# Kernel tuning notes

Hardware: AMD Instinct MI355X
Metric: run time of the kernel (lower is better)

## Reference

```python
import jax, jax.numpy as jnp
import numpy as np

K = 15          # k_point_level
EPS = 1e-5      # BatchNorm eps
NEG = 0.2       # LeakyReLU slope


def _lrelu(y):
    return jnp.where(y > 0, y, NEG * y)


def _knn_idx(x, k):
    # x: [N, C, P] -> idx [N, P, k] of nearest points (incl. self) by -||xi-xj||^2 topk
    inner = -2.0 * jnp.einsum('ncp,ncq->npq', x, x)
    xx = jnp.sum(x * x, axis=1)                      # [N, P]
    pd = -xx[:, :, None] - inner - xx[:, None, :]    # [N, P, P]
    return jax.lax.top_k(pd, k)[1]


def _edge_feature(x, k):
    # x: [N, C, P] -> [N, P, k, 2C] = concat(neigh - center, center)
    N = x.shape[0]
    idx = _knn_idx(x, k)                             # [N, P, k]
    xt = jnp.transpose(x, (0, 2, 1))                 # [N, P, C]
    neigh = xt[jnp.arange(N)[:, None, None], idx]    # [N, P, k, C]
    center = jnp.broadcast_to(xt[:, :, None, :], neigh.shape)
    return jnp.concatenate([neigh - center, center], axis=-1)


def _edge_block(x, W, gamma, beta, k):
    # EdgeConv: gather -> 1x1 conv -> BN (batch stats) -> LeakyReLU -> max over k
    f = _edge_feature(x, k)                          # [N, P, k, 2C]
    y = jnp.einsum('npkc,oc->npko', f, W)
    m = jnp.mean(y, axis=(0, 1, 2))
    v = jnp.var(y, axis=(0, 1, 2))
    y = (y - m) * jax.lax.rsqrt(v + EPS) * gamma + beta
    y = jnp.max(_lrelu(y), axis=2)                   # [N, P, O]
    return jnp.transpose(y, (0, 2, 1))               # [N, O, P]


def _forward(x, W1, g1, b1, W2, g2, b2, W3, g3, b3, W4, g4, b4,
             W5, g5, b5, Wl1, g6, b6, Wl2, bl2, g7, b7, Wl3, bl3):
    x1 = _edge_block(x, W1, g1, b1, K)               # [N, 64, P]
    x2 = _edge_block(x1, W2, g2, b2, K)              # [N, 64, P]
    x3 = _edge_block(x2, W3, g3, b3, K)              # [N, 128, P]
    x4 = _edge_block(x3, W4, g4, b4, K)              # [N, 256, P]
    xc = jnp.concatenate([x1, x2, x3, x4], axis=1)   # [N, 512, P]
    y = jnp.einsum('ncp,oc->npo', xc, W5)            # [N, P, emb]
    m = jnp.mean(y, axis=(0, 1)); v = jnp.var(y, axis=(0, 1))
    y = _lrelu((y - m) * jax.lax.rsqrt(v + EPS) * g5 + b5)
    h = jnp.concatenate([jnp.max(y, axis=1), jnp.mean(y, axis=1)], axis=1)  # [N, 2*emb]
    h = h @ Wl1.T
    m = jnp.mean(h, axis=0); v = jnp.var(h, axis=0)
    h = _lrelu((h - m) * jax.lax.rsqrt(v + EPS) * g6 + b6)
    h = h @ Wl2.T + bl2
    m = jnp.mean(h, axis=0); v = jnp.var(h, axis=0)
    h = _lrelu((h - m) * jax.lax.rsqrt(v + EPS) * g7 + b7)
    logits = h @ Wl3.T + bl3
    return jax.nn.log_softmax(logits, axis=1)


def setup_inputs() -> dict:
    key = jax.random.key(0)
    ks = iter(jax.random.split(key, 16))
    N, P, EMB, NC = 2048, 32, 1024, 800

    def w(k, o, i):
        return jax.random.normal(k, (o, i), jnp.float32) / np.sqrt(i)

    d = {
        'x': jax.random.normal(next(ks), (N, 3, P), jnp.float32),
        'info_point_set': jnp.zeros((1,), jnp.float32),
        'W1': w(next(ks), 64, 6),   'g1': jnp.ones(64),  'b1': jnp.zeros(64),
        'W2': w(next(ks), 64, 128), 'g2': jnp.ones(64),  'b2': jnp.zeros(64),
        'W3': w(next(ks), 128, 128),'g3': jnp.ones(128), 'b3': jnp.zeros(128),
        'W4': w(next(ks), 256, 256),'g4': jnp.ones(256), 'b4': jnp.zeros(256),
        'W5': w(next(ks), EMB, 512),'g5': jnp.ones(EMB), 'b5': jnp.zeros(EMB),
        'Wl1': w(next(ks), 512, 2 * EMB), 'g6': jnp.ones(512), 'b6': jnp.zeros(512),
        'Wl2': w(next(ks), 256, 512), 'bl2': jnp.zeros(256),
        'g7': jnp.ones(256), 'b7': jnp.zeros(256),
        'Wl3': w(next(ks), NC, 256), 'bl3': jnp.zeros(NC),
    }
    return d


def reference(x, info_point_set, W1, g1, b1, W2, g2, b2, W3, g3, b3,
              W4, g4, b4, W5, g5, b5, Wl1, g6, b6, Wl2, bl2, g7, b7, Wl3, bl3):
    # info_point_set unused: args.k + args.k_global == 0 path (dynamic KNN graph).
    return _forward(x, W1, g1, b1, W2, g2, b2, W3, g3, b3, W4, g4, b4,
                    W5, g5, b5, Wl1, g6, b6, Wl2, bl2, g7, b7, Wl3, bl3)
```

## Files before the change

kernel.cpp:

```cpp
#include <hip/hip_runtime.h>
#include <hip/hip_bf16.h>
#include <cstdint>
#include <cstddef>

#define NPTS 2048
#define P 32
#define KNN_K 15
#define LRELU_NEG 0.2f
#define BN_EPS 1e-5f

__device__ __forceinline__ float lrelu(float x) { return x > 0.f ? x : LRELU_NEG * x; }

__device__ __forceinline__ unsigned short f2bf(float x) {
    union { float f; unsigned u; } uu; uu.f = x;
    unsigned r = uu.u + 0x7fffu + ((uu.u >> 16) & 1u);
    return (unsigned short)(r >> 16);
}
__device__ __forceinline__ float bf2f(unsigned short b) {
    union { unsigned u; float f; } uu; uu.u = ((unsigned)b) << 16;
    return uu.f;
}

typedef short bf16x8 __attribute__((ext_vector_type(8)));
typedef float f32x4  __attribute__((ext_vector_type(4)));

template<int C>
__global__ __launch_bounds__(64) void knn_kernel(const float* __restrict__ xin, int cloudStride,
                                                 unsigned char* __restrict__ idx)
{
    const int n = blockIdx.x, t = threadIdx.x;
    __shared__ float xs[C][P];
    __shared__ float xx[P];
    __shared__ float pd[P][P + 1];
    const float* xp = xin + (size_t)n * cloudStride;
    for (int i = t; i < C * P; i += 64) xs[i / P][i % P] = xp[i];
    __syncthreads();
    if (t < P) { float s = 0.f; for (int c = 0; c < C; ++c) { float v = xs[c][t]; s = fmaf(v, v, s); } xx[t] = s; }
    __syncthreads();
    for (int i = t; i < P * P; i += 64) {
        int p = i >> 5, q = i & 31;
        float d = 0.f;
        for (int c = 0; c < C; ++c) d = fmaf(xs[c][p], xs[c][q], d);
        pd[p][q] = 2.f * d - xx[p] - xx[q];
    }
    __syncthreads();
    if (t < P) {
        for (int j = 0; j < KNN_K; ++j) {
            float best = -INFINITY; int bq = 0;
            for (int q = 0; q < P; ++q) { float v = pd[t][q]; if (v > best) { best = v; bq = q; } }
            idx[(size_t)n * (P * KNN_K) + t * KNN_K + j] = (unsigned char)bq;
            pd[t][bq] = -INFINITY;
        }
    }
}

__global__ __launch_bounds__(256) void build_wcat_kernel(const float* __restrict__ W, float* __restrict__ wt,
                                                         int C, int O, int NCHUNK)
{
    int i = blockIdx.x * 256 + threadIdx.x;
    int tot = C * 2 * O;
    if (i >= tot) return;
    int c = i / (2 * O), col = i % (2 * O);
    int O2C = 2 * O / NCHUNK, OC = O / NCHUNK;
    int chunk = col / O2C, cl = col % O2C;
    float v;
    if (cl < OC) { int o = chunk * OC + cl; v = W[(size_t)o * 2 * C + c]; }
    else { int o = chunk * OC + cl - OC; v = W[(size_t)o * 2 * C + C + c] - W[(size_t)o * 2 * C + c]; }
    wt[i] = v;
}

__global__ __launch_bounds__(256) void pack_wcat_direct(const float* __restrict__ W,
                                                        unsigned short* __restrict__ wpk,
                                                        int C, int O, int NCHUNK)
{
    const int TOTC = 2 * O, NTT = TOTC / 16;
    const int O2C = TOTC / NCHUNK, OC = O / NCHUNK;
    int i = blockIdx.x * 256 + threadIdx.x;
    if (i >= C * TOTC) return;
    int j = i & 7, lane = (i >> 3) & 63, rest = i >> 9;
    int ntg = rest % NTT, kb = rest / NTT;
    int k = kb * 32 + (lane >> 4) * 8 + j;
    int col = ntg * 16 + (lane & 15);
    int chunk = col / O2C, cl = col % O2C;
    float v;
    if (cl < OC) { int o = chunk * OC + cl; v = W[(size_t)o * 2 * C + k]; }
    else         { int o = chunk * OC + cl - OC; v = W[(size_t)o * 2 * C + C + k] - W[(size_t)o * 2 * C + k]; }
    unsigned short hi = f2bf(v);
    wpk[(size_t)rest * 1024 + lane * 8 + j] = hi;
    wpk[(size_t)rest * 1024 + 512 + lane * 8 + j] = f2bf(v - bf2f(hi));
}

__global__ __launch_bounds__(256) void pack_wfc_kernel(const float* __restrict__ W,
                                                       unsigned short* __restrict__ wpk,
                                                       int Kk, int Nn, int NTT)
{
    int i = blockIdx.x * 256 + threadIdx.x;
    if (i >= NTT * 16 * Kk) return;
    int j = i & 7, lane = (i >> 3) & 63, rest = i >> 9;
    int ntg = rest % NTT, kb = rest / NTT;
    int k = kb * 32 + (lane >> 4) * 8 + j;
    int col = ntg * 16 + (lane & 15);
    float v = (col < Nn) ? W[(size_t)col * Kk + k] : 0.f;
    unsigned short hi = f2bf(v);
    wpk[(size_t)rest * 1024 + lane * 8 + j] = hi;
    wpk[(size_t)rest * 1024 + 512 + lane * 8 + j] = f2bf(v - bf2f(hi));
}

template<int C, int O, int NCHUNK, bool OUT>
__global__ __launch_bounds__(256) void edge_pass_kernel(
    const float* __restrict__ xin, int cloudStride,
    const float* __restrict__ wt,
    const unsigned char* __restrict__ idx,
    const float* __restrict__ st,
    float* __restrict__ xcout,
    float* __restrict__ partS, float* __restrict__ partQ)
{
    constexpr int TOTC = 2 * O;
    constexpr int O2C = TOTC / NCHUNK;
    constexpr int OC  = O / NCHUNK;
    constexpr int TPC = (O2C >= 256) ? 1 : (256 / O2C);
    constexpr int CPT = (O2C > 256) ? (O2C / 256) : 1;
    constexpr int PP  = P / TPC;
    constexpr int TPO = 256 / OC;
    constexpr int PPo = P / TPO;
    const int n = blockIdx.x, t = threadIdx.x;

    __shared__ float xs[C][P];
    __shared__ float gh[P * O2C];
    __shared__ unsigned char idl[P * KNN_K];
    __shared__ float red[2][256];

    const float* xp = xin + (size_t)n * cloudStride;
    for (int i = t; i < C * P; i += 256) xs[i / P][i % P] = xp[i];
    for (int i = t; i < P * KNN_K; i += 256) idl[i] = idx[(size_t)n * (P * KNN_K) + i];

    const int col = (O2C >= 256) ? t : (t % O2C);
    const int p0  = ((O2C >= 256) ? 0 : (t / O2C)) * PP;
    const int o   = t % OC;
    const int p0c = (t / OC) * PPo;

    for (int chunk = 0; chunk < NCHUNK; ++chunk) {
        __syncthreads();
        {
            float acc[CPT][PP];
            #pragma unroll
            for (int j = 0; j < CPT; ++j)
                #pragma unroll
                for (int p = 0; p < PP; ++p) acc[j][p] = 0.f;
            for (int c = 0; c < C; ++c) {
                float w[CPT];
                #pragma unroll
                for (int j = 0; j < CPT; ++j) w[j] = wt[(size_t)c * TOTC + chunk * O2C + col + j * 256];
                #pragma unroll
                for (int p = 0; p < PP; ++p) {
                    float xv = xs[c][p0 + p];
                    #pragma unroll
                    for (int j = 0; j < CPT; ++j) acc[j][p] = fmaf(w[j], xv, acc[j][p]);
                }
            }
            #pragma unroll
            for (int j = 0; j < CPT; ++j)
                #pragma unroll
                for (int p = 0; p < PP; ++p) gh[(p0 + p) * O2C + col + j * 256] = acc[j][p];
        }
        __syncthreads();

        if constexpr (!OUT) {
            float ssum = 0.f, ssq = 0.f;
            #pragma unroll
            for (int p = 0; p < PPo; ++p) {
                const int pp = p0c + p;
                const float g = gh[pp * O2C + OC + o];
                #pragma unroll
                for (int k = 0; k < KNN_K; ++k) {
                    const int q = idl[pp * KNN_K + k];
                    float yv = gh[q * O2C + o] + g;
                    ssum += yv; ssq += yv * yv;
                }
            }
            red[0][t] = ssum; red[1][t] = ssq;
            __syncthreads();
            if (t < OC) {
                float S = 0.f, Q = 0.f;
                #pragma unroll
                for (int j = 0; j < TPO; ++j) { S += red[0][t + j * OC]; Q += red[1][t + j * OC]; }
                partS[(size_t)(chunk * OC + t) * 2048 + n] = S;
                partQ[(size_t)(chunk * OC + t) * 2048 + n] = Q;
            }
        } else {
            const float s = st[chunk * OC + o], sh = st[1024 + chunk * OC + o];
            float rbuf[PPo];
            #pragma unroll
            for (int p = 0; p < PPo; ++p) {
                const int pp = p0c + p;
                const float g = gh[pp * O2C + OC + o];
                float mx = -INFINITY, mn = INFINITY;
                #pragma unroll
                for (int k = 0; k < KNN_K; ++k) {
                    const int q = idl[pp * KNN_K + k];
                    float yv = gh[q * O2C + o] + g;
                    mx = fmaxf(mx, yv); mn = fminf(mn, yv);
                }
                rbuf[p] = lrelu(fmaf(s, (s >= 0.f ? mx : mn), sh));
            }
            __syncthreads();
            #pragma unroll
            for (int p = 0; p < PPo; ++p) gh[o * (P + 1) + p0c + p] = rbuf[p];
            __syncthreads();
            for (int i = t; i < OC * P; i += 256)
                xcout[(size_t)n * (512 * P) + chunk * OC * P + i] = gh[(i / P) * (P + 1) + (i % P)];
        }
    }
}

template<int C, int O, bool OUT>
__global__ __launch_bounds__(256) void edge_mfma_kernel(
    const float* __restrict__ xin, int cloudStride,
    const unsigned short* __restrict__ wpk,
    const unsigned char* __restrict__ idx,
    const float* __restrict__ st,
    float* __restrict__ xcout,
    float* __restrict__ partS, float* __restrict__ partQ)
{
    constexpr int TOTC  = 2 * O;
    constexpr int O2C   = (TOTC > 256) ? 256 : TOTC;
    constexpr int NCHUNK= TOTC / O2C;
    constexpr int OC    = O2C / 2;
    constexpr int NTW   = O2C / 64;
    constexpr int KB    = C / 32;
    constexpr int NTT   = TOTC / 16;
    constexpr int AS    = C + 8;
    constexpr int GHS   = O2C + 4;
    constexpr int TPO   = 256 / OC;
    constexpr int PPo   = P / TPO;

    const int n = blockIdx.x, t = threadIdx.x;
    const int w = t >> 6, l = t & 63;
    const int lg = l >> 4, lm = l & 15;

    __shared__ unsigned short Ah[P * AS];
    __shared__ unsigned short Al[P * AS];
    __shared__ float gh[P * GHS];
    __shared__ unsigned char idl[P * KNN_K];

    const float* xp = xin + (size_t)n * cloudStride;
    for (int i = t; i < C * P; i += 256) {
        int c = i / P, p = i % P;
        float v = xp[i];
        unsigned short hi = f2bf(v);
        Ah[p * AS + c] = hi;
        Al[p * AS + c] = f2bf(v - bf2f(hi));
    }
    for (int i = t; i < P * KNN_K; i += 256) idl[i] = idx[(size_t)n * (P * KNN_K) + i];
    __syncthreads();

    const int o = t % OC;
    const int p0c = (t / OC) * PPo;

    for (int chunk = 0; chunk < NCHUNK; ++chunk) {
        f32x4 acc[2][NTW];
        #pragma unroll
        for (int mt = 0; mt < 2; ++mt)
            #pragma unroll
            for (int nt = 0; nt < NTW; ++nt) acc[mt][nt] = (f32x4)0.f;

        #pragma unroll
        for (int kb = 0; kb < KB; ++kb) {
            bf16x8 a_h[2], a_l[2];
            #pragma unroll
            for (int mt = 0; mt < 2; ++mt) {
                int row = mt * 16 + lm;
                a_h[mt] = *(const bf16x8*)&Ah[row * AS + kb * 32 + lg * 8];
                a_l[mt] = *(const bf16x8*)&Al[row * AS + kb * 32 + lg * 8];
            }
            #pragma unroll
            for (int nt = 0; nt < NTW; ++nt) {
                int ntg = chunk * (O2C / 16) + w * NTW + nt;
                const unsigned short* bp = wpk + (size_t)(kb * NTT + ntg) * 1024 + (size_t)l * 8;
                bf16x8 Bh = *(const bf16x8*)bp;
                bf16x8 Bl = *(const bf16x8*)(bp + 512);
                #pragma unroll
                for (int mt = 0; mt < 2; ++mt) {
                    acc[mt][nt] = __builtin_amdgcn_mfma_f32_16x16x32_bf16(a_h[mt], Bl, acc[mt][nt], 0, 0, 0);
                    acc[mt][nt] = __builtin_amdgcn_mfma_f32_16x16x32_bf16(a_l[mt], Bh, acc[mt][nt], 0, 0, 0);
                    acc[mt][nt] = __builtin_amdgcn_mfma_f32_16x16x32_bf16(a_h[mt], Bh, acc[mt][nt], 0, 0, 0);
                }
            }
        }
        __syncthreads();
        #pragma unroll
        for (int mt = 0; mt < 2; ++mt)
            #pragma unroll
            for (int nt = 0; nt < NTW; ++nt) {
                int colb = (w * NTW + nt) * 16 + lm;
                #pragma unroll
                for (int r = 0; r < 4; ++r)
                    gh[(mt * 16 + lg * 4 + r) * GHS + colb] = acc[mt][nt][r];
            }
        __syncthreads();

        if constexpr (!OUT) {
            float ssum = 0.f, ssq = 0.f;
            #pragma unroll
            for (int p = 0; p < PPo; ++p) {
                const int pp = p0c + p;
                const float g = gh[pp * GHS + OC + o];
                #pragma unroll
                for (int k = 0; k < KNN_K; ++k) {
                    const int q = idl[pp * KNN_K + k];
                    float yv = gh[q * GHS + o] + g;
                    ssum += yv; ssq += yv * yv;
                }
            }
            __syncthreads();
            gh[t] = ssum; gh[256 + t] = ssq;
            __syncthreads();
            if (t < OC) {
                float S = 0.f, Q = 0.f;
                #pragma unroll
                for (int j = 0; j < TPO; ++j) { S += gh[t + j * OC]; Q += gh[256 + t + j * OC]; }
                partS[(size_t)(chunk * OC + t) * 2048 + n] = S;
                partQ[(size_t)(chunk * OC + t) * 2048 + n] = Q;
            }
        } else {
            const float s = st[chunk * OC + o], sh = st[1024 + chunk * OC + o];
            float rbuf[PPo];
            #pragma unroll
            for (int p = 0; p < PPo; ++p) {
                const int pp = p0c + p;
                const float g = gh[pp * GHS + OC + o];
                float mx = -INFINITY, mn = INFINITY;
                #pragma unroll
                for (int k = 0; k < KNN_K; ++k) {
                    const int q = idl[pp * KNN_K + k];
                    float yv = gh[q * GHS + o] + g;
                    mx = fmaxf(mx, yv); mn = fminf(mn, yv);
                }
                rbuf[p] = lrelu(fmaf(s, (s >= 0.f ? mx : mn), sh));
            }
            __syncthreads();
            #pragma unroll
            for (int p = 0; p < PPo; ++p) gh[o * (P + 1) + p0c + p] = rbuf[p];
            __syncthreads();
            for (int i = t; i < OC * P; i += 256)
                xcout[(size_t)n * (512 * P) + chunk * OC * P + i] = gh[(i / P) * (P + 1) + (i % P)];
        }
    }
}

__global__ __launch_bounds__(256) void reduce_stats_kernel(const float* __restrict__ partS,
                                                           const float* __restrict__ partQ,
                                                           const float* __restrict__ gamma,
                                                           const float* __restrict__ beta,
                                                           float* __restrict__ st, int nparts, float inv_count)
{
    const int o = blockIdx.x, t = threadIdx.x;
    __shared__ float rs[256], rq[256];
    float S = 0.f, Q = 0.f;
    for (int i = t; i < nparts; i += 256) { S += partS[(size_t)o * 2048 + i]; Q += partQ[(size_t)o * 2048 + i]; }
    rs[t] = S; rq[t] = Q; __syncthreads();
    for (int w = 128; w > 0; w >>= 1) { if (t < w) { rs[t] += rs[t + w]; rq[t] += rq[t + w]; } __syncthreads(); }
    if (t == 0) {
        float m = rs[0] * inv_count;
        float v = fmaxf(rq[0] * inv_count - m * m, 0.f);
        float s = gamma[o] * rsqrtf(v + BN_EPS);
        st[o] = s;
        st[1024 + o] = fmaf(-m, s, beta[o]);
    }
}

__global__ __launch_bounds__(256) void pack_w5_kernel(const float* __restrict__ W5, unsigned short* __restrict__ wp)
{
    int i = blockIdx.x * 256 + threadIdx.x;
    if (i >= (1 << 19)) return;
    int j = i & 7, lane = (i >> 3) & 63, nt = (i >> 9) & 63, kb = i >> 15;
    int c = kb * 32 + (lane >> 4) * 8 + j;
    int o = nt * 16 + (lane & 15);
    float f = W5[(size_t)o * 512 + c];
    unsigned short hi = f2bf(f);
    unsigned short lo = f2bf(f - bf2f(hi));
    size_t base = (size_t)(kb * 64 + nt) * 2 * 512 + (size_t)lane * 8 + j;
    wp[base] = hi;
    wp[base + 512] = lo;
}

__global__ __launch_bounds__(512) void conv5_store_kernel(
    const float* xc, const unsigned short* __restrict__ wpack,
    unsigned short* y5,
    float* __restrict__ partS, float* __restrict__ partQ)
{
    const int b = blockIdx.x;
    const int t = threadIdx.x;
    const int w = t >> 6, l = t & 63;
    const int lg = l >> 4, lm = l & 15;

    __shared__ unsigned short Ah[2][64][40];
    __shared__ unsigned short Al[2][64][40];

    f32x4 acc[4][8];
    #pragma unroll
    for (int mt = 0; mt < 4; ++mt)
        #pragma unroll
        for (int nt = 0; nt < 8; ++nt) acc[mt][nt] = (f32x4)0.f;

    const float* xbase = xc + (size_t)(b * 2) * (512 * P);

    const int sp4    = t & 7;
    const int schalf = (t >> 3) & 15;
    const int scloud = (t >> 7) & 1;
    const bool sact  = t < 256;

    auto stage = [&](int kb, int buf) {
        if (sact) {
            const float* src = xbase + (size_t)scloud * (512 * P)
                             + (size_t)(kb * 32 + 2 * schalf) * P + sp4 * 4;
            const float4 v0 = *(const float4*)src;
            const float4 v1 = *(const float4*)(src + P);
            const int r0 = scloud * 32 + sp4 * 4;
            #pragma unroll
            for (int e = 0; e < 4; ++e) {
                float a0 = (&v0.x)[e], a1 = (&v1.x)[e];
                unsigned short h0 = f2bf(a0), h1 = f2bf(a1);
                unsigned short l0 = f2bf(a0 - bf2f(h0)), l1 = f2bf(a1 - bf2f(h1));
                *(unsigned*)&Ah[buf][r0 + e][2 * schalf] = (unsigned)h0 | ((unsigned)h1 << 16);
                *(unsigned*)&Al[buf][r0 + e][2 * schalf] = (unsigned)l0 | ((unsigned)l1 << 16);
            }
        }
    };

    stage(0, 0);
    int cur = 0;
    for (int kb = 0; kb < 16; ++kb) {
        __syncthreads();
        if (kb + 1 < 16) stage(kb + 1, cur ^ 1);

        bf16x8 a_h[4], a_l[4];
        #pragma unroll
        for (int mt = 0; mt < 4; ++mt) {
            int row = mt * 16 + lm;
            a_h[mt] = *(const bf16x8*)&Ah[cur][row][lg * 8];
            a_l[mt] = *(const bf16x8*)&Al[cur][row][lg * 8];
        }
        #pragma unroll
        for (int nt = 0; nt < 8; ++nt) {
            const int ntg = w * 8 + nt;
            const unsigned short* bp = wpack + (size_t)(kb * 64 + ntg) * 2 * 512 + (size_t)l * 8;
            bf16x8 Bh = *(const bf16x8*)bp;
            bf16x8 Bl = *(const bf16x8*)(bp + 512);
            #pragma unroll
            for (int mt = 0; mt < 4; ++mt) {
                acc[mt][nt] = __builtin_amdgcn_mfma_f32_16x16x32_bf16(a_h[mt], Bl, acc[mt][nt], 0, 0, 0);
                acc[mt][nt] = __builtin_amdgcn_mfma_f32_16x16x32_bf16(a_l[mt], Bh, acc[mt][nt], 0, 0, 0);
                acc[mt][nt] = __builtin_amdgcn_mfma_f32_16x16x32_bf16(a_h[mt], Bh, acc[mt][nt], 0, 0, 0);
            }
        }
        cur ^= 1;
    }
    __syncthreads();

    #pragma unroll
    for (int nt = 0; nt < 8; ++nt) {
        float s = 0.f, q = 0.f;
        #pragma unroll
        for (int mt = 0; mt < 4; ++mt)
            #pragma unroll
            for (int r = 0; r < 4; ++r) { float v = acc[mt][nt][r]; s += v; q = fmaf(v, v, q); }
        s += __shfl_xor(s, 16); q += __shfl_xor(q, 16);
        s += __shfl_xor(s, 32); q += __shfl_xor(q, 32);
        if (l < 16) {
            int o = w * 128 + nt * 16 + lm;
            partS[(size_t)o * 2048 + b] = s;
            partQ[(size_t)o * 2048 + b] = q;
        }
        #pragma unroll
        for (int mt = 0; mt < 4; ++mt) {
            unsigned p0 = (unsigned)f2bf(acc[mt][nt][0]) | ((unsigned)f2bf(acc[mt][nt][1]) << 16);
            unsigned p1 = (unsigned)f2bf(acc[mt][nt][2]) | ((unsigned)f2bf(acc[mt][nt][3]) << 16);
            size_t off = ((((size_t)b * 8 + w) * 8 + nt) * 4 + mt) * 64 + l;
            ((uint2*)y5)[off] = make_uint2(p0, p1);
        }
    }
}

__global__ __launch_bounds__(512) void conv5_finish_kernel(
    const unsigned short* __restrict__ y5, const float* __restrict__ st, float* __restrict__ h)
{
    const int b = blockIdx.x, t = threadIdx.x;
    const int w = t >> 6, l = t & 63, lm = l & 15;
    #pragma unroll
    for (int nt = 0; nt < 8; ++nt) {
        const int o = w * 128 + nt * 16 + lm;
        const float sc = st[o], sh = st[1024 + o];
        #pragma unroll
        for (int cloud = 0; cloud < 2; ++cloud) {
            float mx = -INFINITY, sm = 0.f;
            #pragma unroll
            for (int half = 0; half < 2; ++half) {
                const int mt = cloud * 2 + half;
                uint2 pk = ((const uint2*)y5)[((((size_t)b * 8 + w) * 8 + nt) * 4 + mt) * 64 + l];
                #pragma unroll
                for (int r = 0; r < 4; ++r) {
                    unsigned word = (r < 2) ? pk.x : pk.y;
                    unsigned short bits = (unsigned short)((r & 1) ? (word >> 16) : (word & 0xffff));
                    float v = lrelu(fmaf(sc, bf2f(bits), sh));
                    mx = fmaxf(mx, v); sm += v;
                }
            }
            mx = fmaxf(mx, __shfl_xor(mx, 16)); sm += __shfl_xor(sm, 16);
            mx = fmaxf(mx, __shfl_xor(mx, 32)); sm += __shfl_xor(sm, 32);
            if (l < 16) {
                const int n = b * 2 + cloud;
                h[(size_t)n * 2048 + o] = mx;
                h[(size_t)n * 2048 + 1024 + o] = sm * (1.f / 32.f);
            }
        }
    }
}

template<bool BNIN, bool STATS>
__global__ __launch_bounds__(256) void gemm_mfma_nt(
    const float* __restrict__ A, const unsigned short* __restrict__ wpk,
    const float* __restrict__ stbn, const float* __restrict__ bias,
    float* __restrict__ Cc, float* __restrict__ partS, float* __restrict__ partQ,
    int Nn, int NTT, int Kk)
{
    const int o0 = blockIdx.x * 64;
    const int m0 = blockIdx.y * 64;
    const int t = threadIdx.x;
    const int w = t >> 6, l = t & 63;
    const int lg = l >> 4, lm = l & 15;

    __shared__ unsigned short Ah[2][64][40];
    __shared__ unsigned short Al[2][64][40];

    f32x4 acc[4];
    #pragma unroll
    for (int mt = 0; mt < 4; ++mt) acc[mt] = (f32x4)0.f;

    const int srow = t >> 3;
    const int sk4  = (t & 7) * 4;

    auto stage = [&](int kb, int buf) {
        const float* src = A + (size_t)(m0 + srow) * Kk + kb * 32 + sk4;
        float4 v0 = *(const float4*)src;
        float4 v1 = *(const float4*)(src + (size_t)32 * Kk);
        if (BNIN) {
            const float4 s4 = *(const float4*)(stbn + kb * 32 + sk4);
            const float4 t4 = *(const float4*)(stbn + 1024 + kb * 32 + sk4);
            #pragma unroll
            for (int e = 0; e < 4; ++e) {
                (&v0.x)[e] = lrelu(fmaf((&s4.x)[e], (&v0.x)[e], (&t4.x)[e]));
                (&v1.x)[e] = lrelu(fmaf((&s4.x)[e], (&v1.x)[e], (&t4.x)[e]));
            }
        }
        #pragma unroll
        for (int e = 0; e < 4; e += 2) {
            float a0 = (&v0.x)[e], a1 = (&v0.x)[e + 1];
            unsigned short h0 = f2bf(a0), h1 = f2bf(a1);
            *(unsigned*)&Ah[buf][srow][sk4 + e] = (unsigned)h0 | ((unsigned)h1 << 16);
            *(unsigned*)&Al[buf][srow][sk4 + e] =
                (unsigned)f2bf(a0 - bf2f(h0)) | ((unsigned)f2bf(a1 - bf2f(h1)) << 16);
            float b0 = (&v1.x)[e], b1 = (&v1.x)[e + 1];
            unsigned short g0 = f2bf(b0), g1 = f2bf(b1);
            *(unsigned*)&Ah[buf][srow + 32][sk4 + e] = (unsigned)g0 | ((unsigned)g1 << 16);
            *(unsigned*)&Al[buf][srow + 32][sk4 + e] =
                (unsigned)f2bf(b0 - bf2f(g0)) | ((unsigned)f2bf(b1 - bf2f(g1)) << 16);
        }
    };

    const int KB = Kk >> 5;
    stage(0, 0);
    int cur = 0;
    const int ntg = blockIdx.x * 4 + w;
    for (int kb = 0; kb < KB; ++kb) {
        __syncthreads();
        if (kb + 1 < KB) stage(kb + 1, cur ^ 1);
        bf16x8 a_h[4], a_l[4];
        #pragma unroll
        for (int mt = 0; mt < 4; ++mt) {
            a_h[mt] = *(const bf16x8*)&Ah[cur][mt * 16 + lm][lg * 8];
            a_l[mt] = *(const bf16x8*)&Al[cur][mt * 16 + lm][lg * 8];
        }
        const unsigned short* bp = wpk + ((size_t)kb * NTT + ntg) * 1024 + (size_t)l * 8;
        bf16x8 Bh = *(const bf16x8*)bp;
        bf16x8 Bl = *(const bf16x8*)(bp + 512);
        #pragma unroll
        for (int mt = 0; mt < 4; ++mt) {
            acc[mt] = __builtin_amdgcn_mfma_f32_16x16x32_bf16(a_h[mt], Bl, acc[mt], 0, 0, 0);
            acc[mt] = __builtin_amdgcn_mfma_f32_16x16x32_bf16(a_l[mt], Bh, acc[mt], 0, 0, 0);
            acc[mt] = __builtin_amdgcn_mfma_f32_16x16x32_bf16(a_h[mt], Bh, acc[mt], 0, 0, 0);
        }
        cur ^= 1;
    }

    const int col = o0 + w * 16 + lm;
    const bool cok = col < Nn;
    const float bv = (bias != nullptr && cok) ? bias[col] : 0.f;
    float s = 0.f, q = 0.f;
    #pragma unroll
    for (int mt = 0; mt < 4; ++mt) {
        #pragma unroll
        for (int r = 0; r < 4; ++r) {
            float v = acc[mt][r] + bv;
            if (STATS) { s += v; q = fmaf(v, v, q); }
            if (cok) Cc[(size_t)(m0 + mt * 16 + lg * 4 + r) * Nn + col] = v;
        }
    }
    if (STATS) {
        s += __shfl_xor(s, 16); q += __shfl_xor(q, 16);
        s += __shfl_xor(s, 32); q += __shfl_xor(q, 32);
        if (l < 16 && cok) {
            partS[(size_t)col * 2048 + blockIdx.y] = s;
            partQ[(size_t)col * 2048 + blockIdx.y] = q;
        }
    }
}

__global__ __launch_bounds__(256) void logsoftmax_kernel(float* __restrict__ out)
{
    const int n = blockIdx.x, t = threadIdx.x;
    float* row = out + (size_t)n * 800;
    __shared__ float red[256];
    float v[4];
    float mx = -INFINITY;
    #pragma unroll
    for (int j = 0; j < 4; ++j) {
        int i = t + j * 256;
        v[j] = (i < 800) ? row[i] : -INFINITY;
        mx = fmaxf(mx, v[j]);
    }
    red[t] = mx; __syncthreads();
    for (int w = 128; w > 0; w >>= 1) { if (t < w) red[t] = fmaxf(red[t], red[t + w]); __syncthreads(); }
    const float m = red[0]; __syncthreads();
    float s = 0.f;
    #pragma unroll
    for (int j = 0; j < 4; ++j) { int i = t + j * 256; if (i < 800) s += expf(v[j] - m); }
    red[t] = s; __syncthreads();
    for (int w = 128; w > 0; w >>= 1) { if (t < w) red[t] += red[t + w]; __syncthreads(); }
    const float lg = m + logf(red[0]);
    #pragma unroll
    for (int j = 0; j < 4; ++j) { int i = t + j * 256; if (i < 800) row[i] = v[j] - lg; }
}

extern "C" void kernel_launch(void* const* d_in, const int* in_sizes, int n_in,
                              void* d_out, int out_size, void* d_ws, size_t ws_size,
                              hipStream_t stream)
{
    (void)in_sizes; (void)n_in; (void)out_size; (void)ws_size;
    const float* x   = (const float*)d_in[0];
    const float* W1  = (const float*)d_in[2];
    const float* g1  = (const float*)d_in[3];
    const float* b1  = (const float*)d_in[4];
    const float* W2  = (const float*)d_in[5];
    const float* g2  = (const float*)d_in[6];
    const float* b2  = (const float*)d_in[7];
    const float* W3  = (const float*)d_in[8];
    const float* g3  = (const float*)d_in[9];
    const float* b3  = (const float*)d_in[10];
    const float* W4  = (const float*)d_in[11];
    const float* g4  = (const float*)d_in[12];
    const float* b4  = (const float*)d_in[13];
    const float* W5  = (const float*)d_in[14];
    const float* g5  = (const float*)d_in[15];
    const float* b5  = (const float*)d_in[16];
    const float* Wl1 = (const float*)d_in[17];
    const float* g6  = (const float*)d_in[18];
    const float* b6  = (const float*)d_in[19];
    const float* Wl2 = (const float*)d_in[20];
    const float* bl2 = (const float*)d_in[21];
    const float* g7  = (const float*)d_in[22];
    const float* b7  = (const float*)d_in[23];
    const float* Wl3 = (const float*)d_in[24];
    const float* bl3 = (const float*)d_in[25];

    char* ws = (char*)d_ws;
    size_t off = 0;
    auto alloc = [&](size_t bytes) -> void* {
        void* p = ws + off; off += (bytes + 255) & ~(size_t)255; return p;
    };
    float*          xc    = (float*)alloc((size_t)NPTS * 512 * P * 4);
    unsigned char*  idx   = (unsigned char*)alloc((size_t)NPTS * P * KNN_K);
    float*          partS = (float*)alloc((size_t)1024 * 2048 * 4);
    float*          partQ = (float*)alloc((size_t)1024 * 2048 * 4);
    float*          st    = (float*)alloc(2048 * 4);
    float*          wt    = (float*)alloc((size_t)512 * 1024 * 4);
    unsigned short* wpk   = (unsigned short*)alloc((size_t)128 * 512 * 2 * 2);
    unsigned short* fcpk  = (unsigned short*)alloc((size_t)512 * 2048 * 2 * 2);
    float*          h     = (float*)alloc((size_t)2048 * 2048 * 4);
    float*          h1p   = (float*)alloc((size_t)2048 * 512 * 4);
    unsigned short* y5 = (unsigned short*)xc;
    float* h2p = h + 1048576;

    const float inv_edge = 1.f / (float)(NPTS * P * KNN_K);

    knn_kernel<3><<<NPTS, 64, 0, stream>>>(x, 3 * P, idx);
    build_wcat_kernel<<<(3 * 128 + 255) / 256, 256, 0, stream>>>(W1, wt, 3, 64, 1);
    edge_pass_kernel<3, 64, 1, false><<<NPTS, 256, 0, stream>>>(x, 3 * P, wt, idx, nullptr, nullptr, partS, partQ);
    reduce_stats_kernel<<<64, 256, 0, stream>>>(partS, partQ, g1, b1, st, 2048, inv_edge);
    edge_pass_kernel<3, 64, 1, true><<<NPTS, 256, 0, stream>>>(x, 3 * P, wt, idx, st, xc + 0 * P, nullptr, nullptr);

    knn_kernel<64><<<NPTS, 64, 0, stream>>>(xc, 512 * P, idx);
    pack_wcat_direct<<<(64 * 128 + 255) / 256, 256, 0, stream>>>(W2, wpk, 64, 64, 1);
    edge_mfma_kernel<64, 64, false><<<NPTS, 256, 0, stream>>>(xc, 512 * P, wpk, idx, nullptr, nullptr, partS, partQ);
    reduce_stats_kernel<<<64, 256, 0, stream>>>(partS, partQ, g2, b2, st, 2048, inv_edge);
    edge_mfma_kernel<64, 64, true><<<NPTS, 256, 0, stream>>>(xc, 512 * P, wpk, idx, st, xc + 64 * P, nullptr, nullptr);

    knn_kernel<64><<<NPTS, 64, 0, stream>>>(xc + 64 * P, 512 * P, idx);
    pack_wcat_direct<<<(64 * 256 + 255) / 256, 256, 0, stream>>>(W3, wpk, 64, 128, 1);
    edge_mfma_kernel<64, 128, false><<<NPTS, 256, 0, stream>>>(xc + 64 * P, 512 * P, wpk, idx, nullptr, nullptr, partS, partQ);
    reduce_stats_kernel<<<128, 256, 0, stream>>>(partS, partQ, g3, b3, st, 2048, inv_edge);
    edge_mfma_kernel<64, 128, true><<<NPTS, 256, 0, stream>>>(xc + 64 * P, 512 * P, wpk, idx, st, xc + 128 * P, nullptr, nullptr);

    knn_kernel<128><<<NPTS, 64, 0, stream>>>(xc + 128 * P, 512 * P, idx);
    pack_wcat_direct<<<(128 * 512 + 255) / 256, 256, 0, stream>>>(W4, wpk, 128, 256, 2);
    edge_mfma_kernel<128, 256, false><<<NPTS, 256, 0, stream>>>(xc + 128 * P, 512 * P, wpk, idx, nullptr, nullptr, partS, partQ);
    reduce_stats_kernel<<<256, 256, 0, stream>>>(partS, partQ, g4, b4, st, 2048, inv_edge);
    edge_mfma_kernel<128, 256, true><<<NPTS, 256, 0, stream>>>(xc + 128 * P, 512 * P, wpk, idx, st, xc + 256 * P, nullptr, nullptr);

    pack_w5_kernel<<<2048, 256, 0, stream>>>(W5, (unsigned short*)wt);
    conv5_store_kernel<<<1024, 512, 0, stream>>>(xc, (const unsigned short*)wt, y5, partS, partQ);
    reduce_stats_kernel<<<1024, 256, 0, stream>>>(partS, partQ, g5, b5, st, 1024, 1.f / 65536.f);
    conv5_finish_kernel<<<1024, 512, 0, stream>>>(y5, st, h);

    pack_wfc_kernel<<<4096, 256, 0, stream>>>(Wl1, fcpk, 2048, 512, 32);
    gemm_mfma_nt<false, true><<<dim3(8, 32), 256, 0, stream>>>(h, fcpk, nullptr, nullptr, h1p, partS, partQ, 512, 32, 2048);
    reduce_stats_kernel<<<512, 256, 0, stream>>>(partS, partQ, g6, b6, st, 32, 1.f / 2048.f);

    pack_wfc_kernel<<<512, 256, 0, stream>>>(Wl2, fcpk, 512, 256, 16);
    gemm_mfma_nt<true, true><<<dim3(4, 32), 256, 0, stream>>>(h1p, fcpk, st, bl2, h2p, partS, partQ, 256, 16, 512);
    reduce_stats_kernel<<<256, 256, 0, stream>>>(partS, partQ, g7, b7, st, 32, 1.f / 2048.f);

    pack_wfc_kernel<<<832, 256, 0, stream>>>(Wl3, fcpk, 256, 800, 52);
    gemm_mfma_nt<true, false><<<dim3(13, 32), 256, 0, stream>>>(h2p, fcpk, st, bl3, (float*)d_out, nullptr, nullptr, 800, 52, 256);

    logsoftmax_kernel<<<NPTS, 256, 0, stream>>>((float*)d_out);
}
```

Measured before the change: 851.1 us.

## Fuse KNN into first edge pass and merge all weight packing into one launch

The standalone KNN kernels are removed. Neighbour search now runs inside the stats (first) pass of each edge block, using shared memory already allocated there, and writes the indices out for the second pass. All weight-packing kernels are merged into one launch at the start that writes to separate buffers. This removes several launches and a separate read of each activation tensor, but it lengthens the first edge pass and adds work from only 32 threads per block in that pass.

```diff
diff --git a/kernel.cpp b/kernel.cpp
--- a/kernel.cpp
+++ b/kernel.cpp
@@ -24,63 +24,17 @@
 typedef short bf16x8 __attribute__((ext_vector_type(8)));
 typedef float f32x4  __attribute__((ext_vector_type(4)));
 
-template<int C>
-__global__ __launch_bounds__(64) void knn_kernel(const float* __restrict__ xin, int cloudStride,
-                                                 unsigned char* __restrict__ idx)
-{
-    const int n = blockIdx.x, t = threadIdx.x;
-    __shared__ float xs[C][P];
-    __shared__ float xx[P];
-    __shared__ float pd[P][P + 1];
-    const float* xp = xin + (size_t)n * cloudStride;
-    for (int i = t; i < C * P; i += 64) xs[i / P][i % P] = xp[i];
-    __syncthreads();
-    if (t < P) { float s = 0.f; for (int c = 0; c < C; ++c) { float v = xs[c][t]; s = fmaf(v, v, s); } xx[t] = s; }
-    __syncthreads();
-    for (int i = t; i < P * P; i += 64) {
-        int p = i >> 5, q = i & 31;
-        float d = 0.f;
-        for (int c = 0; c < C; ++c) d = fmaf(xs[c][p], xs[c][q], d);
-        pd[p][q] = 2.f * d - xx[p] - xx[q];
-    }
-    __syncthreads();
-    if (t < P) {
-        for (int j = 0; j < KNN_K; ++j) {
-            float best = -INFINITY; int bq = 0;
-            for (int q = 0; q < P; ++q) { float v = pd[t][q]; if (v > best) { best = v; bq = q; } }
-            idx[(size_t)n * (P * KNN_K) + t * KNN_K + j] = (unsigned char)bq;
-            pd[t][bq] = -INFINITY;
-        }
-    }
-}
-
-__global__ __launch_bounds__(256) void build_wcat_kernel(const float* __restrict__ W, float* __restrict__ wt,
-                                                         int C, int O, int NCHUNK)
-{
-    int i = blockIdx.x * 256 + threadIdx.x;
-    int tot = C * 2 * O;
-    if (i >= tot) return;
-    int c = i / (2 * O), col = i % (2 * O);
-    int O2C = 2 * O / NCHUNK, OC = O / NCHUNK;
-    int chunk = col / O2C, cl = col % O2C;
-    float v;
-    if (cl < OC) { int o = chunk * OC + cl; v = W[(size_t)o * 2 * C + c]; }
-    else { int o = chunk * OC + cl - OC; v = W[(size_t)o * 2 * C + C + c] - W[(size_t)o * 2 * C + c]; }
-    wt[i] = v;
-}
-
-__global__ __launch_bounds__(256) void pack_wcat_direct(const float* __restrict__ W,
-                                                        unsigned short* __restrict__ wpk,
-                                                        int C, int O, int NCHUNK)
+__device__ __forceinline__ void edge_pack_body(int i, const float* __restrict__ W,
+                                               unsigned short* __restrict__ wpk,
+                                               int C, int O, int NCHUNK)
 {
     const int TOTC = 2 * O, NTT = TOTC / 16;
-    const int O2C = TOTC / NCHUNK, OC = O / NCHUNK;
-    int i = blockIdx.x * 256 + threadIdx.x;
     if (i >= C * TOTC) return;
     int j = i & 7, lane = (i >> 3) & 63, rest = i >> 9;
     int ntg = rest % NTT, kb = rest / NTT;
     int k = kb * 32 + (lane >> 4) * 8 + j;
     int col = ntg * 16 + (lane & 15);
+    int O2C = TOTC / NCHUNK, OC = O / NCHUNK;
     int chunk = col / O2C, cl = col % O2C;
     float v;
     if (cl < OC) { int o = chunk * OC + cl; v = W[(size_t)o * 2 * C + k]; }
@@ -90,11 +44,10 @@
     wpk[(size_t)rest * 1024 + 512 + lane * 8 + j] = f2bf(v - bf2f(hi));
 }
 
-__global__ __launch_bounds__(256) void pack_wfc_kernel(const float* __restrict__ W,
-                                                       unsigned short* __restrict__ wpk,
-                                                       int Kk, int Nn, int NTT)
-{
-    int i = blockIdx.x * 256 + threadIdx.x;
+__device__ __forceinline__ void wfc_pack_body(int i, const float* __restrict__ W,
+                                              unsigned short* __restrict__ wpk,
+                                              int Kk, int Nn, int NTT)
+{
     if (i >= NTT * 16 * Kk) return;
     int j = i & 7, lane = (i >> 3) & 63, rest = i >> 9;
     int ntg = rest % NTT, kb = rest / NTT;
@@ -106,11 +59,53 @@
     wpk[(size_t)rest * 1024 + 512 + lane * 8 + j] = f2bf(v - bf2f(hi));
 }
 
+__global__ __launch_bounds__(256) void pack_all_kernel(
+    const float* __restrict__ W1, const float* __restrict__ W2,
+    const float* __restrict__ W3, const float* __restrict__ W4,
+    const float* __restrict__ W5, const float* __restrict__ Wl1,
+    const float* __restrict__ Wl2, const float* __restrict__ Wl3,
+    float* __restrict__ wt1,
+    unsigned short* __restrict__ wpk2, unsigned short* __restrict__ wpk3,
+    unsigned short* __restrict__ wpk4, unsigned short* __restrict__ w5pk,
+    unsigned short* __restrict__ fc1pk, unsigned short* __restrict__ fc2pk,
+    unsigned short* __restrict__ fc3pk)
+{
+    const int b = blockIdx.x, t = threadIdx.x;
+    if (b < 2) {
+        int i = b * 256 + t;
+        if (i < 3 * 128) {
+            int c = i / 128, col = i % 128;
+            float v;
+            if (col < 64) v = W1[(size_t)col * 6 + c];
+            else          v = W1[(size_t)(col - 64) * 6 + 3 + c] - W1[(size_t)(col - 64) * 6 + c];
+            wt1[i] = v;
+        }
+    } else if (b < 34)   edge_pack_body((b - 2)    * 256 + t, W2, wpk2, 64, 64, 1);
+    else if (b < 98)     edge_pack_body((b - 34)   * 256 + t, W3, wpk3, 64, 128, 1);
+    else if (b < 354)    edge_pack_body((b - 98)   * 256 + t, W4, wpk4, 128, 256, 2);
+    else if (b < 2402) {
+        int i = (b - 354) * 256 + t;
+        if (i < (1 << 19)) {
+            int j = i & 7, lane = (i >> 3) & 63, nt = (i >> 9) & 63, kb = i >> 15;
+            int c = kb * 32 + (lane >> 4) * 8 + j;
+            int o = nt * 16 + (lane & 15);
+            float f = W5[(size_t)o * 512 + c];
+            unsigned short hi = f2bf(f);
+            size_t base = (size_t)(kb * 64 + nt) * 1024 + (size_t)lane * 8 + j;
+            w5pk[base] = hi;
+            w5pk[base + 512] = f2bf(f - bf2f(hi));
+        }
+    }
+    else if (b < 6498)   wfc_pack_body((b - 2402) * 256 + t, Wl1, fc1pk, 2048, 512, 32);
+    else if (b < 7010)   wfc_pack_body((b - 6498) * 256 + t, Wl2, fc2pk, 512, 256, 16);
+    else                 wfc_pack_body((b - 7010) * 256 + t, Wl3, fc3pk, 256, 800, 52);
+}
+
 template<int C, int O, int NCHUNK, bool OUT>
 __global__ __launch_bounds__(256) void edge_pass_kernel(
     const float* __restrict__ xin, int cloudStride,
     const float* __restrict__ wt,
-    const unsigned char* __restrict__ idx,
+    unsigned char* idx,
     const float* __restrict__ st,
     float* __restrict__ xcout,
     float* __restrict__ partS, float* __restrict__ partQ)
@@ -129,10 +124,35 @@
     __shared__ float gh[P * O2C];
     __shared__ unsigned char idl[P * KNN_K];
     __shared__ float red[2][256];
+    __shared__ float xx[P];
 
     const float* xp = xin + (size_t)n * cloudStride;
     for (int i = t; i < C * P; i += 256) xs[i / P][i % P] = xp[i];
-    for (int i = t; i < P * KNN_K; i += 256) idl[i] = idx[(size_t)n * (P * KNN_K) + i];
+
+    if constexpr (!OUT) {
+        float* pd = gh;
+        __syncthreads();
+        if (t < P) { float s = 0.f; for (int c = 0; c < C; ++c) { float v = xs[c][t]; s = fmaf(v, v, s); } xx[t] = s; }
+        __syncthreads();
+        for (int i = t; i < P * P; i += 256) {
+            int p = i >> 5, q = i & 31;
+            float d = 0.f;
+            for (int c = 0; c < C; ++c) d = fmaf(xs[c][p], xs[c][q], d);
+            pd[p * (P + 1) + q] = 2.f * d - xx[p] - xx[q];
+        }
+        __syncthreads();
+        if (t < P) {
+            for (int j = 0; j < KNN_K; ++j) {
+                float best = -INFINITY; int bq = 0;
+                for (int q = 0; q < P; ++q) { float v = pd[t * (P + 1) + q]; if (v > best) { best = v; bq = q; } }
+                idl[t * KNN_K + j] = (unsigned char)bq;
+                idx[(size_t)n * (P * KNN_K) + t * KNN_K + j] = (unsigned char)bq;
+                pd[t * (P + 1) + bq] = -INFINITY;
+            }
+        }
+    } else {
+        for (int i = t; i < P * KNN_K; i += 256) idl[i] = idx[(size_t)n * (P * KNN_K) + i];
+    }
 
     const int col = (O2C >= 256) ? t : (t % O2C);
     const int p0  = ((O2C >= 256) ? 0 : (t / O2C)) * PP;
@@ -217,7 +237,7 @@
 __global__ __launch_bounds__(256) void edge_mfma_kernel(
     const float* __restrict__ xin, int cloudStride,
     const unsigned short* __restrict__ wpk,
-    const unsigned char* __restrict__ idx,
+    unsigned char* idx,
     const float* __restrict__ st,
     float* __restrict__ xcout,
     float* __restrict__ partS, float* __restrict__ partQ)
@@ -233,6 +253,7 @@
     constexpr int GHS   = O2C + 4;
     constexpr int TPO   = 256 / OC;
     constexpr int PPo   = P / TPO;
+    static_assert(P * GHS >= C * P + P * (P + 1), "pd+xs must fit in gh");
 
     const int n = blockIdx.x, t = threadIdx.x;
     const int w = t >> 6, l = t & 63;
@@ -242,17 +263,51 @@
     __shared__ unsigned short Al[P * AS];
     __shared__ float gh[P * GHS];
     __shared__ unsigned char idl[P * KNN_K];
+    __shared__ float xx[P];
 
     const float* xp = xin + (size_t)n * cloudStride;
-    for (int i = t; i < C * P; i += 256) {
-        int c = i / P, p = i % P;
-        float v = xp[i];
-        unsigned short hi = f2bf(v);
-        Ah[p * AS + c] = hi;
-        Al[p * AS + c] = f2bf(v - bf2f(hi));
-    }
-    for (int i = t; i < P * KNN_K; i += 256) idl[i] = idx[(size_t)n * (P * KNN_K) + i];
-    __syncthreads();
+    if constexpr (!OUT) {
+        float* xsf = gh;
+        float* pd  = gh + C * P;
+        for (int i = t; i < C * P; i += 256) {
+            int c = i / P, p = i % P;
+            float v = xp[i];
+            unsigned short hi = f2bf(v);
+            Ah[p * AS + c] = hi;
+            Al[p * AS + c] = f2bf(v - bf2f(hi));
+            xsf[i] = v;
+        }
+        __syncthreads();
+        if (t < P) { float s = 0.f; for (int c = 0; c < C; ++c) { float v = xsf[c * P + t]; s = fmaf(v, v, s); } xx[t] = s; }
+        __syncthreads();
+        for (int i = t; i < P * P; i += 256) {
+            int p = i >> 5, q = i & 31;
+            float d = 0.f;
+            for (int c = 0; c < C; ++c) d = fmaf(xsf[c * P + p], xsf[c * P + q], d);
+            pd[p * (P + 1) + q] = 2.f * d - xx[p] - xx[q];
+        }
+        __syncthreads();
+        if (t < P) {
+            for (int j = 0; j < KNN_K; ++j) {
+                float best = -INFINITY; int bq = 0;
+                for (int q = 0; q < P; ++q) { float v = pd[t * (P + 1) + q]; if (v > best) { best = v; bq = q; } }
+                idl[t * KNN_K + j] = (unsigned char)bq;
+                idx[(size_t)n * (P * KNN_K) + t * KNN_K + j] = (unsigned char)bq;
+                pd[t * (P + 1) + bq] = -INFINITY;
+            }
+        }
+        __syncthreads();
+    } else {
+        for (int i = t; i < C * P; i += 256) {
+            int c = i / P, p = i % P;
+            float v = xp[i];
+            unsigned short hi = f2bf(v);
+            Ah[p * AS + c] = hi;
+            Al[p * AS + c] = f2bf(v - bf2f(hi));
+        }
+        for (int i = t; i < P * KNN_K; i += 256) idl[i] = idx[(size_t)n * (P * KNN_K) + i];
+        __syncthreads();
+    }
 
     const int o = t % OC;
     const int p0c = (t / OC) * PPo;
@@ -367,21 +422,6 @@
         st[o] = s;
         st[1024 + o] = fmaf(-m, s, beta[o]);
     }
-}
-
-__global__ __launch_bounds__(256) void pack_w5_kernel(const float* __restrict__ W5, unsigned short* __restrict__ wp)
-{
-    int i = blockIdx.x * 256 + threadIdx.x;
-    if (i >= (1 << 19)) return;
-    int j = i & 7, lane = (i >> 3) & 63, nt = (i >> 9) & 63, kb = i >> 15;
-    int c = kb * 32 + (lane >> 4) * 8 + j;
-    int o = nt * 16 + (lane & 15);
-    float f = W5[(size_t)o * 512 + c];
-    unsigned short hi = f2bf(f);
-    unsigned short lo = f2bf(f - bf2f(hi));
-    size_t base = (size_t)(kb * 64 + nt) * 2 * 512 + (size_t)lane * 8 + j;
-    wp[base] = hi;
-    wp[base + 512] = lo;
 }
 
 __global__ __launch_bounds__(512) void conv5_store_kernel(
@@ -683,9 +723,14 @@
     float*          partS = (float*)alloc((size_t)1024 * 2048 * 4);
     float*          partQ = (float*)alloc((size_t)1024 * 2048 * 4);
     float*          st    = (float*)alloc(2048 * 4);
-    float*          wt    = (float*)alloc((size_t)512 * 1024 * 4);
-    unsigned short* wpk   = (unsigned short*)alloc((size_t)128 * 512 * 2 * 2);
-    unsigned short* fcpk  = (unsigned short*)alloc((size_t)512 * 2048 * 2 * 2);
+    float*          wt1   = (float*)alloc(3 * 128 * 4);
+    unsigned short* wpk2  = (unsigned short*)alloc((size_t)2 * 64 * 128 * 2);
+    unsigned short* wpk3  = (unsigned short*)alloc((size_t)2 * 64 * 256 * 2);
+    unsigned short* wpk4  = (unsigned short*)alloc((size_t)2 * 128 * 512 * 2);
+    unsigned short* w5pk  = (unsigned short*)alloc((size_t)2 * 512 * 1024 * 2);
+    unsigned short* fc1pk = (unsigned short*)alloc((size_t)2 * 512 * 2048 * 2);
+    unsigned short* fc2pk = (unsigned short*)alloc((size_t)2 * 256 * 512 * 2);
+    unsigned short* fc3pk = (unsigned short*)alloc((size_t)2 * 832 * 256 * 2);
     float*          h     = (float*)alloc((size_t)2048 * 2048 * 4);
     float*          h1p   = (float*)alloc((size_t)2048 * 512 * 4);
     unsigned short* y5 = (unsigned short*)xc;
@@ -693,45 +738,36 @@
 
     const float inv_edge = 1.f / (float)(NPTS * P * KNN_K);
 
-    knn_kernel<3><<<NPTS, 64, 0, stream>>>(x, 3 * P, idx);
-    build_wcat_kernel<<<(3 * 128 + 255) / 256, 256, 0, stream>>>(W1, wt, 3, 64, 1);
-    edge_pass_kernel<3, 64, 1, false><<<NPTS, 256, 0, stream>>>(x, 3 * P, wt, idx, nullptr, nullptr, partS, partQ);
+    pack_all_kernel<<<7842, 256, 0, stream>>>(W1, W2, W3, W4, W5, Wl1, Wl2, Wl3,
+                                              wt1, wpk2, wpk3, wpk4, w5pk, fc1pk, fc2pk, fc3pk);
+
+    edge_pass_kernel<3, 64, 1, false><<<NPTS, 256, 0, stream>>>(x, 3 * P, wt1, idx, nullptr, nullptr, partS, partQ);
     reduce_stats_kernel<<<64, 256, 0, stream>>>(partS, partQ, g1, b1, st, 2048, inv_edge);
-    edge_pass_kernel<3, 64, 1, true><<<NPTS, 256, 0, stream>>>(x, 3 * P, wt, idx, st, xc + 0 * P, nullptr, nullptr);
-
-    knn_kernel<64><<<NPTS, 64, 0, stream>>>(xc, 512 * P, idx);
-    pack_wcat_direct<<<(64 * 128 + 255) / 256, 256, 0, stream>>>(W2, wpk, 64, 64, 1);
-    edge_mfma_kernel<64, 64, false><<<NPTS, 256, 0, stream>>>(xc, 512 * P, wpk, idx, nullptr, nullptr, partS, partQ);
+    edge_pass_kernel<3, 64, 1, true><<<NPTS, 256, 0, stream>>>(x, 3 * P, wt1, idx, st, xc + 0 * P, nullptr, nullptr);
+
+    edge_mfma_kernel<64, 64, false><<<NPTS, 256, 0, stream>>>(xc, 512 * P, wpk2, idx, nullptr, nullptr, partS, partQ);
     reduce_stats_kernel<<<64, 256, 0, stream>>>(partS, partQ, g2, b2, st, 2048, inv_edge);
-    edge_mfma_kernel<64, 64, true><<<NPTS, 256, 0, stream>>>(xc, 512 * P, wpk, idx, st, xc + 64 * P, nullptr, nullptr);
-
-    knn_kernel<64><<<NPTS, 64, 0, stream>>>(xc + 64 * P, 512 * P, idx);
-    pack_wcat_direct<<<(64 * 256 + 255) / 256, 256, 0, stream>>>(W3, wpk, 64, 128, 1);
-    edge_mfma_kernel<64, 128, false><<<NPTS, 256, 0, stream>>>(xc + 64 * P, 512 * P, wpk, idx, nullptr, nullptr, partS, partQ);
+    edge_mfma_kernel<64, 64, true><<<NPTS, 256, 0, stream>>>(xc, 512 * P, wpk2, idx, st, xc + 64 * P, nullptr, nullptr);
+
+    edge_mfma_kernel<64, 128, false><<<NPTS, 256, 0, stream>>>(xc + 64 * P, 512 * P, wpk3, idx, nullptr, nullptr, partS, partQ);
     reduce_stats_kernel<<<128, 256, 0, stream>>>(partS, partQ, g3, b3, st, 2048, inv_edge);
-    edge_mfma_kernel<64, 128, true><<<NPTS, 256, 0, stream>>>(xc + 64 * P, 512 * P, wpk, idx, st, xc + 128 * P, nullptr, nullptr);
-
-    knn_kernel<128><<<NPTS, 64, 0, stream>>>(xc + 128 * P, 512 * P, idx);
-    pack_wcat_direct<<<(128 * 512 + 255) / 256, 256, 0, stream>>>(W4, wpk, 128, 256, 2);
-    edge_mfma_kernel<128, 256, false><<<NPTS, 256, 0, stream>>>(xc + 128 * P, 512 * P, wpk, idx, nullptr, nullptr, partS, partQ);
+    edge_mfma_kernel<64, 128, true><<<NPTS, 256, 0, stream>>>(xc + 64 * P, 512 * P, wpk3, idx, st, xc + 128 * P, nullptr, nullptr);
+
+    edge_mfma_kernel<128, 256, false><<<NPTS, 256, 0, stream>>>(xc + 128 * P, 512 * P, wpk4, idx, nullptr, nullptr, partS, partQ);
     reduce_stats_kernel<<<256, 256, 0, stream>>>(partS, partQ, g4, b4, st, 2048, inv_edge);
-    edge_mfma_kernel<128, 256, true><<<NPTS, 256, 0, stream>>>(xc + 128 * P, 512 * P, wpk, idx, st, xc + 256 * P, nullptr, nullptr);
-
-    pack_w5_kernel<<<2048, 256, 0, stream>>>(W5, (unsigned short*)wt);
-    conv5_store_kernel<<<1024, 512, 0, stream>>>(xc, (const unsigned short*)wt, y5, partS, partQ);
+    edge_mfma_kernel<128, 256, true><<<NPTS, 256, 0, stream>>>(xc + 128 * P, 512 * P, wpk4, idx, st, xc + 256 * P, nullptr, nullptr);
+
+    conv5_store_kernel<<<1024, 512, 0, stream>>>(xc, w5pk, y5, partS, partQ);
     reduce_stats_kernel<<<1024, 256, 0, stream>>>(partS, partQ, g5, b5, st, 1024, 1.f / 65536.f);
     conv5_finish_kernel<<<1024, 512, 0, stream>>>(y5, st, h);
 
-    pack_wfc_kernel<<<4096, 256, 0, stream>>>(Wl1, fcpk, 2048, 512, 32);
-    gemm_mfma_nt<false, true><<<dim3(8, 32), 256, 0, stream>>>(h, fcpk, nullptr, nullptr, h1p, partS, partQ, 512, 32, 2048);
+    gemm_mfma_nt<false, true><<<dim3(8, 32), 256, 0, stream>>>(h, fc1pk, nullptr, nullptr, h1p, partS, partQ, 512, 32, 2048);
     reduce_stats_kernel<<<512, 256, 0, stream>>>(partS, partQ, g6, b6, st, 32, 1.f / 2048.f);
 
-    pack_wfc_kernel<<<512, 256, 0, stream>>>(Wl2, fcpk, 512, 256, 16);
-    gemm_mfma_nt<true, true><<<dim3(4, 32), 256, 0, stream>>>(h1p, fcpk, st, bl2, h2p, partS, partQ, 256, 16, 512);
+    gemm_mfma_nt<true, true><<<dim3(4, 32), 256, 0, stream>>>(h1p, fc2pk, st, bl2, h2p, partS, partQ, 256, 16, 512);
     reduce_stats_kernel<<<256, 256, 0, stream>>>(partS, partQ, g7, b7, st, 32, 1.f / 2048.f);
 
-    pack_wfc_kernel<<<832, 256, 0, stream>>>(Wl3, fcpk, 256, 800, 52);
-    gemm_mfma_nt<true, false><<<dim3(13, 32), 256, 0, stream>>>(h2p, fcpk, st, bl3, (float*)d_out, nullptr, nullptr, 800, 52, 256);
+    gemm_mfma_nt<true, false><<<dim3(13, 32), 256, 0, stream>>>(h2p, fc3pk, st, bl3, (float*)d_out, nullptr, nullptr, 800, 52, 256);
 
     logsoftmax_kernel<<<NPTS, 256, 0, stream>>>((float*)d_out);
 }
```

Measured after the change: 849.9 us. About the same (-0.1%).
